# Kernel optimization log

Measured on AMD Instinct MI355X. Metric: run time of the kernel, lower is better.

## Reference

```python
import jax, jax.numpy as jnp
import numpy as np
import math

HID, H = 384, 4
D = HID // H  # 96, HGT head dim
N_T = [2048, 2048, 2048, 1024, 1024]  # user_turn, ai_turn, stance, pressure, belief
OFF = [0, 2048, 4096, 6144, 7168]
NTOT = 8192
# (src_type, dst_type, num_edges)
EDGES = [(0, 1, 32768), (1, 0, 32768), (1, 2, 32768), (2, 2, 32768),
         (0, 3, 16384), (3, 1, 32768), (1, 4, 16384), (4, 2, 32768)]
E_OFF = np.concatenate([[0], np.cumsum([c for _, _, c in EDGES])]).tolist()


def _gelu(x):
    return jax.nn.gelu(x, approximate=False)


def _ln(x, g, b, eps=1e-5):
    m = x.mean(-1, keepdims=True)
    v = ((x - m) ** 2).mean(-1, keepdims=True)
    return (x - m) * jax.lax.rsqrt(v + eps) * g + b


def _mha(q_in, kv_in, Wqkv, bqkv, Wo, bo):
    # torch nn.MultiheadAttention (batch_first, batch=1); Wqkv stored [E, 3E]
    E = HID
    q = (q_in @ Wqkv[:, :E] + bqkv[:E]).reshape(-1, H, D)
    k = (kv_in @ Wqkv[:, E:2 * E] + bqkv[E:2 * E]).reshape(-1, H, D)
    v = (kv_in @ Wqkv[:, 2 * E:] + bqkv[2 * E:]).reshape(-1, H, D)
    s = jnp.einsum('qhd,khd->hqk', q, k) / math.sqrt(D)
    w = jax.nn.softmax(s, axis=-1)
    o = jnp.einsum('hqk,khd->qhd', w, v).reshape(-1, E)
    return o @ Wo + bo


def _forward(x_user, x_ai, x_stance, x_pressure, x_belief,
             hgt_Wkqv, hgt_bkqv, hgt_Wout, hgt_bout, hgt_krel, hgt_vrel, hgt_prel, hgt_skip,
             ln_g, ln_b, sp_W, sp_b, sp_lng, sp_lnb, fc0_W, fc0_b, bn_g, bn_b,
             tq_W, tq_b, tk_W, tk_b, tv_W, tv_b, mha_Wqkv, mha_bqkv, mha_Wo, mha_bo,
             c1_W, c1_b, c2_W, c2_b, op_W, op_b, as1_W, as1_b, as2_W, as2_b,
             sc1_W, sc1_b, sc2_W, sc2_b, cl1_W, cl1_b, cl_lng, cl_lnb,
             cl2_W, cl2_b, cl3_W, cl3_b, tp_W, tp_b, edge_src, edge_dst):
    xs = [x_user, x_ai, x_stance, x_pressure, x_belief]
    for l in range(2):
        kqv = [x @ hgt_Wkqv[l, t] + hgt_bkqv[l, t] for t, x in enumerate(xs)]
        kk = [a[:, :HID].reshape(-1, H, D) for a in kqv]
        qq = [a[:, HID:2 * HID].reshape(-1, H, D) for a in kqv]
        vv = [a[:, 2 * HID:].reshape(-1, H, D) for a in kqv]
        al, msg, dgl = [], [], []
        for r, (s, d, cnt) in enumerate(EDGES):
            si = edge_src[E_OFF[r]:E_OFF[r + 1]]
            di = edge_dst[E_OFF[r]:E_OFF[r + 1]]
            ke = jnp.einsum('ehd,hdf->ehf', kk[s][si], hgt_krel[l, r])
            ve = jnp.einsum('ehd,hdf->ehf', vv[s][si], hgt_vrel[l, r])
            a = (qq[d][di] * ke).sum(-1) * hgt_prel[l, r] / math.sqrt(D)  # [E_r, H]
            al.append(a); msg.append(ve); dgl.append(di + OFF[d])
        a = jnp.concatenate(al); ve = jnp.concatenate(msg); dg = jnp.concatenate(dgl)
        mx = jax.ops.segment_max(a, dg, num_segments=NTOT)
        ex = jnp.exp(a - mx[dg])
        den = jax.ops.segment_sum(ex, dg, num_segments=NTOT)
        w = ex / den[dg]
        agg = jax.ops.segment_sum(ve * w[:, :, None], dg, num_segments=NTOT).reshape(NTOT, HID)
        new = []
        for t, x in enumerate(xs):
            o = _gelu(agg[OFF[t]:OFF[t] + N_T[t]]) @ hgt_Wout[l, t] + hgt_bout[l, t]
            g = jax.nn.sigmoid(hgt_skip[l, t])
            new.append(g * o + (1 - g) * x)
        xs = [_ln(_gelu(v), ln_g[t], ln_b[t]) for t, v in enumerate(new)]
    user_h, ai_h, stance_h, pressure_h, belief_h = xs

    # ---- StanceTrajectoryEncoder ----
    hs = _gelu(_ln(stance_h @ sp_W + sp_b, sp_lng, sp_lnb))

    def bn(x, i):  # eval-mode BatchNorm1d, running stats (0, 1)
        return x * (bn_g[i] / math.sqrt(1.0 + 1e-5)) + bn_b[i]

    xg = jax.nn.relu(bn(hs @ fc0_W + fc0_b, 0))
    Ns = hs.shape[0]
    for i in range(2):  # SGFormer TransConv layers (linear global attention)
        q = (xg @ tq_W[i] + tq_b[i]).reshape(Ns, H, HID)
        k = (xg @ tk_W[i] + tk_b[i]).reshape(Ns, H, HID)
        v = (xg @ tv_W[i] + tv_b[i]).reshape(Ns, H, HID)
        qn = q / jnp.linalg.norm(q)  # global Frobenius norm, as in SGFormer
        kn = k / jnp.linalg.norm(k)
        kvs = jnp.einsum('lhm,lhd->hmd', kn, v)
        num = jnp.einsum('nhm,hmd->nhd', qn, kvs) + Ns * v
        dnm = jnp.einsum('nhm,hm->nh', qn, kn.sum(0))[:, :, None] + Ns
        z = (num / dnm).mean(axis=1)  # mean over heads
        xg = jax.nn.relu(bn(0.5 * z + 0.5 * xg, i + 1))  # residual alpha=0.5
    h_mixed = 0.7 * hs + 0.3 * xg
    traj = _mha(h_mixed, h_mixed, mha_Wqkv[1], mha_bqkv[1], mha_Wo[1], mha_bo[1])
    traj_summary = traj.mean(0, keepdims=True)  # [1, HID]
    ci = h_mixed.T[None]  # [1, C, L]
    dn = ('NCH', 'OIH', 'NCH')
    c = jax.lax.conv_general_dilated(ci, c1_W, (1,), [(1, 1)], dimension_numbers=dn) + c1_b[None, :, None]
    c = _gelu(c)
    c = jax.lax.conv_general_dilated(c, c2_W, (1,), [(1, 1)], dimension_numbers=dn) + c2_b[None, :, None]
    c = _gelu(c)
    decay_summary = c.mean(axis=2)  # [1, HID//2]
    traj_emb = jnp.concatenate([traj_summary, decay_summary], -1) @ op_W + op_b

    # ---- PressureResponseModule ----
    ai_ctx = _mha(ai_h, user_h, mha_Wqkv[0], mha_bqkv[0], mha_Wo[0], mha_bo[0])
    ml = min(N_T[1], N_T[0])
    comb = jnp.concatenate([ai_h[:ml], user_h[:ml]], -1)
    pscores = jax.nn.sigmoid((jax.nn.relu(comb @ as1_W + as1_b) @ as2_W + as2_b)[:, 0])
    ai_pooled = ai_ctx.mean(0, keepdims=True)

    # ---- belief attention + stance comparison + classifier ----
    bctx = _mha(ai_h, belief_h, mha_Wqkv[2], mha_bqkv[2], mha_Wo[2], mha_bo[2]).mean(0, keepdims=True)
    sd_in = jnp.concatenate([stance_h[0:1], stance_h[-1:]], -1)
    stance_delta = jax.nn.relu(sd_in @ sc1_W + sc1_b) @ sc2_W + sc2_b
    comb2 = jnp.concatenate([traj_emb, ai_pooled, bctx, stance_delta], -1)  # [1, 1344]
    z = jax.nn.relu(_ln(comb2 @ cl1_W + cl1_b, cl_lng, cl_lnb))
    z = jax.nn.relu(z @ cl2_W + cl2_b)
    logits = (z @ cl3_W + cl3_b).reshape(())
    decay = jax.nn.sigmoid(logits)
    per_turn = jax.nn.sigmoid((ai_ctx @ tp_W + tp_b)[:, 0])
    return logits, decay, per_turn, pscores


def setup_inputs() -> dict:
    key = jax.random.key(0)
    ks = iter(jax.random.split(key, 128))

    def P(shape, fan_in):
        return jax.random.normal(next(ks), shape, jnp.float32) / np.float32(math.sqrt(fan_in))

    inp = {}
    for name, n in zip(['x_user', 'x_ai', 'x_stance', 'x_pressure', 'x_belief'], N_T):
        inp[name] = jax.random.normal(next(ks), (n, HID), jnp.float32)
    inp['hgt_Wkqv'] = P((2, 5, HID, 3 * HID), HID)
    inp['hgt_bkqv'] = jnp.zeros((2, 5, 3 * HID))
    inp['hgt_Wout'] = P((2, 5, HID, HID), HID)
    inp['hgt_bout'] = jnp.zeros((2, 5, HID))
    inp['hgt_krel'] = P((2, 8, H, D, D), D)
    inp['hgt_vrel'] = P((2, 8, H, D, D), D)
    inp['hgt_prel'] = jnp.ones((2, 8, H))
    inp['hgt_skip'] = jnp.ones((2, 5))
    inp['ln_g'] = jnp.ones((5, HID)); inp['ln_b'] = jnp.zeros((5, HID))
    inp['sp_W'] = P((HID, HID), HID); inp['sp_b'] = jnp.zeros((HID,))
    inp['sp_lng'] = jnp.ones((HID,)); inp['sp_lnb'] = jnp.zeros((HID,))
    inp['fc0_W'] = P((HID, HID), HID); inp['fc0_b'] = jnp.zeros((HID,))
    inp['bn_g'] = jnp.ones((3, HID)); inp['bn_b'] = jnp.zeros((3, HID))
    for nm in ['tq', 'tk', 'tv']:
        inp[nm + '_W'] = P((2, HID, H * HID), HID)
        inp[nm + '_b'] = jnp.zeros((2, H * HID))
    inp['mha_Wqkv'] = P((3, HID, 3 * HID), HID)
    inp['mha_bqkv'] = jnp.zeros((3, 3 * HID))
    inp['mha_Wo'] = P((3, HID, HID), HID)
    inp['mha_bo'] = jnp.zeros((3, HID))
    inp['c1_W'] = P((HID, HID, 3), HID * 3); inp['c1_b'] = jnp.zeros((HID,))
    inp['c2_W'] = P((HID // 2, HID, 3), HID * 3); inp['c2_b'] = jnp.zeros((HID // 2,))
    inp['op_W'] = P((HID + HID // 2, HID), HID + HID // 2); inp['op_b'] = jnp.zeros((HID,))
    inp['as1_W'] = P((2 * HID, HID), 2 * HID); inp['as1_b'] = jnp.zeros((HID,))
    inp['as2_W'] = P((HID, 1), HID); inp['as2_b'] = jnp.zeros((1,))
    inp['sc1_W'] = P((2 * HID, HID), 2 * HID); inp['sc1_b'] = jnp.zeros((HID,))
    inp['sc2_W'] = P((HID, HID // 2), HID); inp['sc2_b'] = jnp.zeros((HID // 2,))
    CIN = 3 * HID + HID // 2
    inp['cl1_W'] = P((CIN, HID), CIN); inp['cl1_b'] = jnp.zeros((HID,))
    inp['cl_lng'] = jnp.ones((HID,)); inp['cl_lnb'] = jnp.zeros((HID,))
    inp['cl2_W'] = P((HID, HID // 2), HID); inp['cl2_b'] = jnp.zeros((HID // 2,))
    inp['cl3_W'] = P((HID // 2, 1), HID // 2); inp['cl3_b'] = jnp.zeros((1,))
    inp['tp_W'] = P((HID, 1), HID); inp['tp_b'] = jnp.zeros((1,))
    srcs, dsts = [], []
    for (s, d, cnt) in EDGES:
        srcs.append(jax.random.randint(next(ks), (cnt,), 0, N_T[s], jnp.int32))
        dsts.append(jax.random.randint(next(ks), (cnt,), 0, N_T[d], jnp.int32))
    inp['edge_src'] = jnp.concatenate(srcs)
    inp['edge_dst'] = jnp.concatenate(dsts)
    return inp


def reference(x_user, x_ai, x_stance, x_pressure, x_belief,
              hgt_Wkqv, hgt_bkqv, hgt_Wout, hgt_bout, hgt_krel, hgt_vrel, hgt_prel, hgt_skip,
              ln_g, ln_b, sp_W, sp_b, sp_lng, sp_lnb, fc0_W, fc0_b, bn_g, bn_b,
              tq_W, tq_b, tk_W, tk_b, tv_W, tv_b, mha_Wqkv, mha_bqkv, mha_Wo, mha_bo,
              c1_W, c1_b, c2_W, c2_b, op_W, op_b, as1_W, as1_b, as2_W, as2_b,
              sc1_W, sc1_b, sc2_W, sc2_b, cl1_W, cl1_b, cl_lng, cl_lnb,
              cl2_W, cl2_b, cl3_W, cl3_b, tp_W, tp_b, edge_src, edge_dst):
    return _forward(x_user, x_ai, x_stance, x_pressure, x_belief,
                    hgt_Wkqv, hgt_bkqv, hgt_Wout, hgt_bout, hgt_krel, hgt_vrel, hgt_prel, hgt_skip,
                    ln_g, ln_b, sp_W, sp_b, sp_lng, sp_lnb, fc0_W, fc0_b, bn_g, bn_b,
                    tq_W, tq_b, tk_W, tk_b, tv_W, tv_b, mha_Wqkv, mha_bqkv, mha_Wo, mha_bo,
                    c1_W, c1_b, c2_W, c2_b, op_W, op_b, as1_W, as1_b, as2_W, as2_b,
                    sc1_W, sc1_b, sc2_W, sc2_b, cl1_W, cl1_b, cl_lng, cl_lnb,
                    cl2_W, cl2_b, cl3_W, cl3_b, tp_W, tp_b, edge_src, edge_dst)
```

## Files before the change

### kernel.cpp

```cpp
#include <hip/hip_runtime.h>
#include <hip/hip_bf16.h>

#define NEDGE 229376
#define NTOT  8192
#define BNCONST 0.9999950000374997f
#define ISQ96   0.10206207261596575f

__constant__ int c_NT[5]     = {2048,2048,2048,1024,1024};
__constant__ int c_OFFS[5]   = {0,2048,4096,6144,7168};
__constant__ int c_ESRC[8]   = {0,1,1,2,0,3,1,4};
__constant__ int c_EDST[8]   = {1,0,2,2,3,1,4,2};
__constant__ int c_EOFF[9]   = {0,32768,65536,98304,131072,147456,180224,196608,229376};
__constant__ int c_RELROW[8] = {0,2048,4096,6144,8192,10240,11264,13312};

static const int h_NT[5]   = {2048,2048,2048,1024,1024};
static const int h_OFFS[5] = {0,2048,4096,6144,7168};

__device__ inline float gelu_f(float x){ return 0.5f*x*(1.0f+erff(x*0.70710678118654752f)); }
__device__ inline float sigm(float x){ return 1.0f/(1.0f+expf(-x)); }
__device__ inline float wsum64(float v){
  #pragma unroll
  for (int s=32;s>0;s>>=1) v += __shfl_xor(v, s, 64);
  return v;
}
__device__ inline unsigned encf(float f){
  unsigned b = __float_as_uint(f);
  return (b & 0x80000000u) ? ~b : (b | 0x80000000u);
}
__device__ inline float decf(unsigned u){
  unsigned b = (u & 0x80000000u) ? (u & 0x7FFFFFFFu) : ~u;
  return __uint_as_float(b);
}
__device__ inline int row_type(int row){
  return (row<2048)?0:((row<4096)?1:((row<6144)?2:((row<7168)?3:4)));
}
__device__ inline float rgmax(float v){
  v = fmaxf(v, __shfl_xor(v, 1, 64));
  v = fmaxf(v, __shfl_xor(v, 2, 64));
  v = fmaxf(v, __shfl_xor(v, 4, 64));
  v = fmaxf(v, __shfl_xor(v, 8, 64));
  return v;
}
__device__ inline float rgsum(float v){
  v += __shfl_xor(v, 1, 64);
  v += __shfl_xor(v, 2, 64);
  v += __shfl_xor(v, 4, 64);
  v += __shfl_xor(v, 8, 64);
  return v;
}


__global__ void k_mix(const float* __restrict__ a, const float* __restrict__ b,
                      float* __restrict__ c, int n, float fa, float fb){
  int i = blockIdx.x*256 + threadIdx.x;
  if (i < n) c[i] = fa*a[i] + fb*b[i];
}

__global__ void k_comb(const float* __restrict__ ai, const float* __restrict__ user,
                       float* __restrict__ cb){
  int i = blockIdx.x*256 + threadIdx.x;
  if (i >= 2048*768) return;
  int n = i / 768, c = i - n*768;
  cb[i] = (c < 384) ? ai[n*384 + c] : user[n*384 + (c-384)];
}


__global__ void k_edge_pre(const int* __restrict__ esrc, const int* __restrict__ edst,
                           int* edg, int* esr, int* erl, int* cnt){
  int e = blockIdx.x*256 + threadIdx.x;
  if (e >= NEDGE) return;
  int r = 0;
  #pragma unroll
  for (int q=1;q<8;q++) if (e >= c_EOFF[q]) r = q;
  int dg = c_OFFS[c_EDST[r]] + edst[e];
  edg[e] = dg;
  esr[e] = c_RELROW[r] + esrc[e];
  erl[e] = r;
  atomicAdd(&cnt[dg], 1);
}

__global__ __launch_bounds__(1024) void k_scan(const int* __restrict__ cnt, int* __restrict__ off){
  __shared__ int sh[1024];
  int tid = threadIdx.x;
  int base = tid*8;
  int loc[8]; int run = 0;
  #pragma unroll
  for (int i=0;i<8;i++){ loc[i] = run; run += cnt[base+i]; }
  sh[tid] = run;
  __syncthreads();
  for (int d=1; d<1024; d<<=1){
    int v = (tid >= d) ? sh[tid-d] : 0;
    __syncthreads();
    sh[tid] += v;
    __syncthreads();
  }
  int pre = (tid==0) ? 0 : sh[tid-1];
  #pragma unroll
  for (int i=0;i<8;i++) off[base+i] = pre + loc[i];
  if (tid==1023) off[8192] = sh[1023];
}

__global__ void k_scatter(const int* __restrict__ edg, const int* __restrict__ off,
                          int* cnt2, int* csr){
  int e = blockIdx.x*256 + threadIdx.x;
  if (e >= NEDGE) return;
  int dg = edg[e];
  int pos = off[dg] + atomicAdd(&cnt2[dg], 1);
  csr[pos] = e;
}


__global__ __launch_bounds__(256) void gemm_f(
    const float* __restrict__ A, int lda, const float* __restrict__ B, int ldb,
    const float* __restrict__ bias, const float* __restrict__ cs, const float* __restrict__ csh,
    float kmul, float* __restrict__ C, int ldc, int M, int N, int K, int act, int agelu)
{
  __shared__ float As[2][16][68];
  __shared__ float Bs[2][16][68];
  int tid = threadIdx.x;
  int tx = tid & 15, ty = tid >> 4;
  int am = tid >> 2, ak = (tid & 3) * 4;
  int bk = tid >> 4, bn = (tid & 15) * 4;
  int m0 = blockIdx.y * 64, n0 = blockIdx.x * 64;
  int gmA = m0 + am;
  int gnB = n0 + bn;
  int ntiles = K >> 4;
  float4 ra, rb;
  float acc[4][4] = {};

  auto fetch = [&](int kk){
    if (gmA < M){
      ra = *reinterpret_cast<const float4*>(&A[(size_t)gmA*lda + kk + ak]);
      if (agelu){ ra.x=gelu_f(ra.x); ra.y=gelu_f(ra.y); ra.z=gelu_f(ra.z); ra.w=gelu_f(ra.w); }
    } else ra = make_float4(0.f,0.f,0.f,0.f);
    if (gnB + 3 < N){
      rb = *reinterpret_cast<const float4*>(&B[(size_t)(kk + bk)*ldb + gnB]);
    } else {
      rb.x = (gnB   < N) ? B[(size_t)(kk + bk)*ldb + gnB  ] : 0.f;
      rb.y = (gnB+1 < N) ? B[(size_t)(kk + bk)*ldb + gnB+1] : 0.f;
      rb.z = (gnB+2 < N) ? B[(size_t)(kk + bk)*ldb + gnB+2] : 0.f;
      rb.w = (gnB+3 < N) ? B[(size_t)(kk + bk)*ldb + gnB+3] : 0.f;
    }
  };
  auto stage = [&](int b){
    As[b][ak  ][am] = ra.x;
    As[b][ak+1][am] = ra.y;
    As[b][ak+2][am] = ra.z;
    As[b][ak+3][am] = ra.w;
    *reinterpret_cast<float4*>(&Bs[b][bk][bn]) = rb;
  };

  fetch(0);
  stage(0);
  __syncthreads();
  for (int t = 0; t < ntiles; t++){
    int cur = t & 1;
    if (t + 1 < ntiles) fetch((t+1) << 4);
    #pragma unroll
    for (int k = 0; k < 16; k++) {
      float4 a4 = *reinterpret_cast<const float4*>(&As[cur][k][ty*4]);
      float4 b4 = *reinterpret_cast<const float4*>(&Bs[cur][k][tx*4]);
      float a[4] = {a4.x, a4.y, a4.z, a4.w};
      float b[4] = {b4.x, b4.y, b4.z, b4.w};
      #pragma unroll
      for (int i=0;i<4;i++)
        #pragma unroll
        for (int j=0;j<4;j++) acc[i][j] += a[i]*b[j];
    }
    if (t + 1 < ntiles) stage(cur ^ 1);
    __syncthreads();
  }
  #pragma unroll
  for (int i=0;i<4;i++){
    int gm = m0 + ty*4 + i; if (gm >= M) continue;
    #pragma unroll
    for (int j=0;j<4;j++){
      int gn = n0 + tx*4 + j; if (gn >= N) continue;
      float v = acc[i][j];
      if (bias) v += bias[gn];
      float s = kmul;
      if (cs) s *= cs[gn];
      v *= s;
      if (csh) v += csh[gn];
      if (act==1) v = fmaxf(v, 0.f);
      else if (act==2) v = gelu_f(v);
      C[(size_t)gm*ldc + gn] = v;
    }
  }
}

__global__ __launch_bounds__(256) void gemm_rel(
    const float* __restrict__ KQV_, const float* __restrict__ krel_l,
    const float* __restrict__ vrel_l, float* __restrict__ KE_, float* __restrict__ VE_)
{
  int z = blockIdx.z;
  int w = z & 1, h = (z >> 1) & 3, r = z >> 3;
  int s = c_ESRC[r];
  int Ns = c_NT[s];
  int m0 = blockIdx.y * 64;
  if (m0 >= Ns) return;
  int n0 = blockIdx.x * 64;
  const float* A = KQV_ + (size_t)c_OFFS[s]*1152 + (w ? 768 : 0) + h*96;
  const float* B = (w ? vrel_l : krel_l) + (size_t)(r*4 + h)*9216;
  float* C = (w ? VE_ : KE_) + (size_t)c_RELROW[r]*384 + h*96;

  __shared__ float As[2][16][68];
  __shared__ float Bs[2][16][68];
  int tid = threadIdx.x;
  int tx = tid & 15, ty = tid >> 4;
  int am = tid >> 2, ak = (tid & 3) * 4;
  int bk = tid >> 4, bn = (tid & 15) * 4;
  int gmA = m0 + am;
  int gnB = n0 + bn;
  float4 ra, rb;
  float acc[4][4] = {};

  auto fetch = [&](int kk){
    ra = (gmA < Ns) ? *reinterpret_cast<const float4*>(&A[(size_t)gmA*1152 + kk + ak])
                    : make_float4(0.f,0.f,0.f,0.f);
    if (gnB + 3 < 96){
      rb = *reinterpret_cast<const float4*>(&B[(size_t)(kk + bk)*96 + gnB]);
    } else {
      rb.x = (gnB   < 96) ? B[(size_t)(kk + bk)*96 + gnB  ] : 0.f;
      rb.y = (gnB+1 < 96) ? B[(size_t)(kk + bk)*96 + gnB+1] : 0.f;
      rb.z = (gnB+2 < 96) ? B[(size_t)(kk + bk)*96 + gnB+2] : 0.f;
      rb.w = (gnB+3 < 96) ? B[(size_t)(kk + bk)*96 + gnB+3] : 0.f;
    }
  };
  auto stage = [&](int b){
    As[b][ak  ][am] = ra.x;
    As[b][ak+1][am] = ra.y;
    As[b][ak+2][am] = ra.z;
    As[b][ak+3][am] = ra.w;
    *reinterpret_cast<float4*>(&Bs[b][bk][bn]) = rb;
  };

  fetch(0);
  stage(0);
  __syncthreads();
  for (int t = 0; t < 6; t++){
    int cur = t & 1;
    if (t + 1 < 6) fetch((t+1) << 4);
    #pragma unroll
    for (int k = 0; k < 16; k++) {
      float4 a4 = *reinterpret_cast<const float4*>(&As[cur][k][ty*4]);
      float4 b4 = *reinterpret_cast<const float4*>(&Bs[cur][k][tx*4]);
      float a[4] = {a4.x, a4.y, a4.z, a4.w};
      float b[4] = {b4.x, b4.y, b4.z, b4.w};
      #pragma unroll
      for (int i=0;i<4;i++)
        #pragma unroll
        for (int j=0;j<4;j++) acc[i][j] += a[i]*b[j];
    }
    if (t + 1 < 6) stage(cur ^ 1);
    __syncthreads();
  }
  #pragma unroll
  for (int i=0;i<4;i++){
    int gm = m0 + ty*4 + i; if (gm >= Ns) continue;
    #pragma unroll
    for (int j=0;j<4;j++){
      int gn = n0 + tx*4 + j; if (gn >= 96) continue;
      C[(size_t)gm*384 + gn] = acc[i][j];
    }
  }
}

__global__ __launch_bounds__(256) void gemm_atb_ks(
    const float* __restrict__ A0, int lda, const float* __restrict__ B0, int ldb,
    float* __restrict__ C0, int ldc, int M, int N, int L,
    int hsA, int hsB, int hsC, int nch)
{
  __shared__ float As[2][16][68];
  __shared__ float Bs[2][16][68];
  int h = blockIdx.z / nch, c = blockIdx.z % nch;
  const float* A = A0 + (size_t)h*hsA;
  const float* B = B0 + (size_t)h*hsB;
  float* C = C0 + (size_t)h*hsC;
  int l0 = c*256;
  int tid = threadIdx.x;
  int tx = tid & 15, ty = tid >> 4;
  int sl = tid >> 4, sq = (tid & 15) * 4;
  int m0 = blockIdx.y * 64, n0 = blockIdx.x * 64;
  int gmA = m0 + sq, gnB = n0 + sq;
  int ntiles = 16;
  float4 ra, rb;
  float acc[4][4] = {};

  auto fetch = [&](int ll){
    if (gmA + 3 < M){
      ra = *reinterpret_cast<const float4*>(&A[(size_t)(ll + sl)*lda + gmA]);
    } else {
      ra.x = (gmA   < M) ? A[(size_t)(ll + sl)*lda + gmA  ] : 0.f;
      ra.y = (gmA+1 < M) ? A[(size_t)(ll + sl)*lda + gmA+1] : 0.f;
      ra.z = (gmA+2 < M) ? A[(size_t)(ll + sl)*lda + gmA+2] : 0.f;
      ra.w = (gmA+3 < M) ? A[(size_t)(ll + sl)*lda + gmA+3] : 0.f;
    }
    if (gnB + 3 < N){
      rb = *reinterpret_cast<const float4*>(&B[(size_t)(ll + sl)*ldb + gnB]);
    } else {
      rb.x = (gnB   < N) ? B[(size_t)(ll + sl)*ldb + gnB  ] : 0.f;
      rb.y = (gnB+1 < N) ? B[(size_t)(ll + sl)*ldb + gnB+1] : 0.f;
      rb.z = (gnB+2 < N) ? B[(size_t)(ll + sl)*ldb + gnB+2] : 0.f;
      rb.w = (gnB+3 < N) ? B[(size_t)(ll + sl)*ldb + gnB+3] : 0.f;
    }
  };
  auto stage = [&](int b){
    *reinterpret_cast<float4*>(&As[b][sl][sq]) = ra;
    *reinterpret_cast<float4*>(&Bs[b][sl][sq]) = rb;
  };

  fetch(l0);
  stage(0);
  __syncthreads();
  for (int t = 0; t < ntiles; t++){
    int cur = t & 1;
    if (t + 1 < ntiles) fetch(l0 + ((t+1) << 4));
    #pragma unroll
    for (int l = 0; l < 16; l++) {
      float4 a4 = *reinterpret_cast<const float4*>(&As[cur][l][ty*4]);
      float4 b4 = *reinterpret_cast<const float4*>(&Bs[cur][l][tx*4]);
      float a[4] = {a4.x, a4.y, a4.z, a4.w};
      float b[4] = {b4.x, b4.y, b4.z, b4.w};
      #pragma unroll
      for (int i=0;i<4;i++)
        #pragma unroll
        for (int j=0;j<4;j++) acc[i][j] += a[i]*b[j];
    }
    if (t + 1 < ntiles) stage(cur ^ 1);
    __syncthreads();
  }
  #pragma unroll
  for (int i=0;i<4;i++){
    int gm = m0 + ty*4 + i; if (gm >= M) continue;
    #pragma unroll
    for (int j=0;j<4;j++){
      int gn = n0 + tx*4 + j; if (gn >= N) continue;
      atomicAdd(&C[(size_t)gm*ldc + gn], acc[i][j]);
    }
  }
}

__global__ __launch_bounds__(256) void fa_kernel(
    const float* __restrict__ MQ, int nq, float* __restrict__ OP, float* __restrict__ ML)
{
  __shared__ float Qs[96][68];
  __shared__ float Ksf[96][36];
  __shared__ float Vs[32][104];
  __shared__ float Ps[64][36];
  int tid = threadIdx.x;
  int tx = tid & 15, ty = tid >> 4;
  int q0 = blockIdx.x * 64;
  int h = blockIdx.y;
  int z = blockIdx.z, nch = gridDim.z;
  int kvbase = z * 512;

  #pragma unroll
  for (int i = 0; i < 6; i++){
    int e = tid + i*256;
    int r = e & 63, kq = (e >> 6) * 4;
    float4 f = *reinterpret_cast<const float4*>(&MQ[(size_t)(q0+r)*1152 + h*96 + kq]);
    Qs[kq  ][r] = f.x;
    Qs[kq+1][r] = f.y;
    Qs[kq+2][r] = f.z;
    Qs[kq+3][r] = f.w;
  }

  float m_i[4], l_i[4], acc[4][6];
  #pragma unroll
  for (int i=0;i<4;i++){
    m_i[i] = -3.0e38f; l_i[i] = 0.f;
    #pragma unroll
    for (int c=0;c<6;c++) acc[i][c] = 0.f;
  }
  int c0 = tx*6;
  __syncthreads();

  for (int t = 0; t < 16; t++){
    int kv0 = kvbase + t*32;
    #pragma unroll
    for (int i = 0; i < 3; i++){
      int e = tid + i*256;
      int n = e & 31, kq = (e >> 5) * 4;
      float4 f = *reinterpret_cast<const float4*>(&MQ[(size_t)(kv0+n)*1152 + 384 + h*96 + kq]);
      Ksf[kq  ][n] = f.x;
      Ksf[kq+1][n] = f.y;
      Ksf[kq+2][n] = f.z;
      Ksf[kq+3][n] = f.w;
      int nv = e / 24, cq = (e - nv*24) * 4;
      float4 g = *reinterpret_cast<const float4*>(&MQ[(size_t)(kv0+nv)*1152 + 768 + h*96 + cq]);
      *reinterpret_cast<float4*>(&Vs[nv][cq]) = g;
    }
    __syncthreads();

    float s0[4] = {0,0,0,0}, s1[4] = {0,0,0,0};
    #pragma unroll 8
    for (int k = 0; k < 96; k++){
      float4 a4 = *reinterpret_cast<const float4*>(&Qs[k][ty*4]);
      float2 b2 = *reinterpret_cast<const float2*>(&Ksf[k][tx*2]);
      s0[0] += a4.x*b2.x; s1[0] += a4.x*b2.y;
      s0[1] += a4.y*b2.x; s1[1] += a4.y*b2.y;
      s0[2] += a4.z*b2.x; s1[2] += a4.z*b2.y;
      s0[3] += a4.w*b2.x; s1[3] += a4.w*b2.y;
    }
    #pragma unroll
    for (int i=0;i<4;i++){
      float a = s0[i]*ISQ96, b = s1[i]*ISQ96;
      float rm = rgmax(fmaxf(a, b));
      float mn = fmaxf(m_i[i], rm);
      float alpha = expf(m_i[i] - mn);
      float p0 = expf(a - mn), p1 = expf(b - mn);
      float rs = rgsum(p0 + p1);
      l_i[i] = l_i[i]*alpha + rs;
      m_i[i] = mn;
      #pragma unroll
      for (int c=0;c<6;c++) acc[i][c] *= alpha;
      Ps[ty*4+i][tx*2  ] = p0;
      Ps[ty*4+i][tx*2+1] = p1;
    }
    __syncthreads();
    for (int kv = 0; kv < 32; kv++){
      float2 v01 = *reinterpret_cast<const float2*>(&Vs[kv][c0]);
      float2 v23 = *reinterpret_cast<const float2*>(&Vs[kv][c0+2]);
      float2 v45 = *reinterpret_cast<const float2*>(&Vs[kv][c0+4]);
      #pragma unroll
      for (int i=0;i<4;i++){
        float p = Ps[ty*4+i][kv];
        acc[i][0] += p*v01.x; acc[i][1] += p*v01.y;
        acc[i][2] += p*v23.x; acc[i][3] += p*v23.y;
        acc[i][4] += p*v45.x; acc[i][5] += p*v45.y;
      }
    }
    __syncthreads();
  }

  size_t base = ((size_t)(h*nch + z)*nq + q0);
  #pragma unroll
  for (int i=0;i<4;i++){
    size_t row = base + ty*4 + i;
    #pragma unroll
    for (int c=0;c<6;c++) OP[row*96 + c0 + c] = acc[i][c];
    if (tx == 0){
      ML[row*2  ] = m_i[i];
      ML[row*2+1] = l_i[i];
    }
  }
}

__global__ void k_famerge(const float* __restrict__ OP, const float* __restrict__ ML,
                          float* __restrict__ AO_, int nq, int nch){
  int e = blockIdx.x*256 + threadIdx.x;
  int total = 4*nq*96;
  if (e >= total) return;
  int c = e % 96;
  int q = (e / 96) % nq;
  int h = e / (96*nq);
  float M = -3.0e38f;
  for (int z = 0; z < nch; z++)
    M = fmaxf(M, ML[((size_t)(h*nch+z)*nq + q)*2]);
  float L = 0.f, O = 0.f;
  for (int z = 0; z < nch; z++){
    size_t row = (size_t)(h*nch+z)*nq + q;
    float w = expf(ML[row*2] - M);
    L += ML[row*2+1]*w;
    O += OP[row*96 + c]*w;
  }
  AO_[(size_t)q*384 + h*96 + c] = O / L;
}

__global__ void k_im2col(const float* __restrict__ in, float* __restrict__ imc){
  int e = blockIdx.x*256 + threadIdx.x;
  if (e >= 2048*1152) return;
  int p = e / 1152, k = e - p*1152;
  int ic = k / 3, j = k - ic*3;
  int gp = p - 1 + j;
  imc[e] = (gp >= 0 && gp < 2048) ? in[(size_t)gp*384 + ic] : 0.f;
}
__global__ void k_wtr(const float* __restrict__ W, float* __restrict__ WT, int OC){
  int e = blockIdx.x*256 + threadIdx.x;
  if (e >= OC*1152) return;
  int oc = e / 1152, k = e - oc*1152;
  WT[(size_t)k*OC + oc] = W[e];
}


__global__ __launch_bounds__(256) void k_escore(
    const float* __restrict__ KQV_, const float* __restrict__ KE_,
    const int* __restrict__ edg, const int* __restrict__ esr, const int* __restrict__ erl,
    const float* __restrict__ prel_l, float* __restrict__ EA)
// ... 68 lines not shown
    const float* __restrict__ O, float* __restrict__ X,
    const float* __restrict__ skip_l, const float* __restrict__ lng, const float* __restrict__ lnb)
{
  __shared__ float red[2];
  int row = blockIdx.x, tid = threadIdx.x;
  int t = row_type(row);
  float gt = sigm(skip_l[t]);
  const float* o = O + (size_t)row*384;
  float* x = X + (size_t)row*384;
  float v0 = gelu_f(gt*o[tid]     + (1.f-gt)*x[tid]);
  float v1 = gelu_f(gt*o[tid+128] + (1.f-gt)*x[tid+128]);
  float v2 = gelu_f(gt*o[tid+256] + (1.f-gt)*x[tid+256]);
  int lane = tid & 63, wid = tid >> 6;
  float s = wsum64(v0+v1+v2);
  if (lane==0) red[wid] = s;
  __syncthreads();
  float mean = (red[0]+red[1]) * (1.0f/384.0f);
  __syncthreads();
  float d0=v0-mean, d1=v1-mean, d2=v2-mean;
  float q = wsum64(d0*d0+d1*d1+d2*d2);
  if (lane==0) red[wid] = q;
  __syncthreads();
  float var = (red[0]+red[1]) * (1.0f/384.0f);
  float rs = 1.0f/sqrtf(var + 1e-5f);
  const float* g = lng + (size_t)t*384;
  const float* b = lnb + (size_t)t*384;
  x[tid]     = d0*rs*g[tid]     + b[tid];
  x[tid+128] = d1*rs*g[tid+128] + b[tid+128];
  x[tid+256] = d2*rs*g[tid+256] + b[tid+256];
}

__global__ __launch_bounds__(128) void k_lnrow(
    const float* __restrict__ X, float* __restrict__ Y,
    const float* __restrict__ g, const float* __restrict__ b, int act)
{
  __shared__ float red[2];
  int row = blockIdx.x, tid = threadIdx.x;
  const float* x = X + (size_t)row*384;
  float* y = Y + (size_t)row*384;
  float v0 = x[tid], v1 = x[tid+128], v2 = x[tid+256];
  int lane = tid & 63, wid = tid >> 6;
  float s = wsum64(v0+v1+v2);
  if (lane==0) red[wid] = s;
  __syncthreads();
  float mean = (red[0]+red[1]) * (1.0f/384.0f);
  __syncthreads();
  float d0=v0-mean, d1=v1-mean, d2=v2-mean;
  float q = wsum64(d0*d0+d1*d1+d2*d2);
  if (lane==0) red[wid] = q;
  __syncthreads();
  float var = (red[0]+red[1]) * (1.0f/384.0f);
  float rs = 1.0f/sqrtf(var + 1e-5f);
  float u0 = d0*rs*g[tid]     + b[tid];
  float u1 = d1*rs*g[tid+128] + b[tid+128];
  float u2 = d2*rs*g[tid+256] + b[tid+256];
  if (act==1){ u0=fmaxf(u0,0.f); u1=fmaxf(u1,0.f); u2=fmaxf(u2,0.f); }
  else       { u0=gelu_f(u0); u1=gelu_f(u1); u2=gelu_f(u2); }
  y[tid] = u0; y[tid+128] = u1; y[tid+256] = u2;
}


__global__ __launch_bounds__(256) void k_sumsq(const float* __restrict__ x, int n, float* out){
  __shared__ float red[4];
  float s = 0.f;
  for (int i = blockIdx.x*256 + threadIdx.x; i < n; i += gridDim.x*256){ float v=x[i]; s += v*v; }
  s = wsum64(s);
  int lane = threadIdx.x & 63, wid = threadIdx.x >> 6;
  if (lane==0) red[wid] = s;
  __syncthreads();
  if (threadIdx.x==0) atomicAdd(out, red[0]+red[1]+red[2]+red[3]);
}

__global__ void k_colsum(const float* __restrict__ A, int R, int C, float scale,
                         float* __restrict__ out){
  int col = blockIdx.x*256 + threadIdx.x;
  if (col >= C) return;
  int nchunk = gridDim.y;
  int chunk = (R + nchunk - 1)/nchunk;
  int r0 = blockIdx.y*chunk, r1 = min(R, r0+chunk);
  float s = 0.f;
  for (int r=r0; r<r1; r++) s += A[(size_t)r*C + col];
  atomicAdd(&out[col], s*scale);
}

__global__ __launch_bounds__(256) void k_dnm(const float* __restrict__ QB,
    const float* __restrict__ KSUM, const float* __restrict__ sqsk, float* __restrict__ DNM){
  int wv = blockIdx.x*4 + (threadIdx.x>>6);
  int n = wv >> 2, h = wv & 3;
  int lane = threadIdx.x & 63;
  const float* q = QB + (size_t)n*1536 + h*384;
  const float* ks = KSUM + h*384;
  float p = 0.f;
  #pragma unroll
  for (int d=lane; d<384; d+=64) p += q[d]*ks[d];
  p = wsum64(p);
  if (lane==0) DNM[n*4+h] = p * (1.0f/sqrtf(sqsk[0]*sqsk[1])) + 2048.0f;
}

__global__ void k_zcomb(const float* __restrict__ ZN, const float* __restrict__ VB_,
                        const float* __restrict__ DNM_, const float* __restrict__ sqsk,
                        float* __restrict__ XG_,
                        const float* __restrict__ bng, const float* __restrict__ bnb){
  int i = blockIdx.x*256 + threadIdx.x;
  if (i >= 2048*384) return;
  int n = i / 384, c = i - n*384;
  float inv_s = 1.0f/sqrtf(sqsk[0]*sqsk[1]);
  float zm = 0.f;
  #pragma unroll
  for (int h=0;h<4;h++){
    float num = ZN[(size_t)n*1536 + h*384 + c]*inv_s + 2048.0f*VB_[(size_t)n*1536 + h*384 + c];
    zm += num / DNM_[n*4+h];
  }
  zm *= 0.25f;
  float y = 0.5f*zm + 0.5f*XG_[i];
  y = y * (bng[c] * BNCONST) + bnb[c];
  XG_[i] = fmaxf(y, 0.f);
}


__global__ __launch_bounds__(256) void k_gemv_ks(
    const float* __restrict__ in, int K, const float* __restrict__ W, int ldw,
    float* __restrict__ tmp, int N)
{
  int c = blockIdx.x*64 + (threadIdx.x & 63);
  int w = threadIdx.x >> 6;
  int kch = blockIdx.y, nk = gridDim.y;
  int k0 = (int)(((long long)K * kch) / nk);
  int k1 = (int)(((long long)K * (kch+1)) / nk);
  float s = 0.f;
  if (c < N){
    for (int k = k0 + w; k < k1; k += 4)
      s += in[k] * W[(size_t)k*ldw + c];
  }
  __shared__ float red[4][64];
  red[w][threadIdx.x & 63] = s;
  __syncthreads();
  if (w == 0 && c < N){
    int l = threadIdx.x & 63;
    tmp[(size_t)kch*N + c] = red[0][l] + red[1][l] + red[2][l] + red[3][l];
  }
}

__global__ void k_gemv_fin(const float* __restrict__ tmp, int nk,
                           const float* __restrict__ b, float* __restrict__ out, int N, int act){
  int c = blockIdx.x*256 + threadIdx.x;
  if (c >= N) return;
  float v = 0.f;
  for (int i = 0; i < nk; i++) v += tmp[(size_t)i*N + c];
  v += b[c];
  if (act==1) v = fmaxf(v, 0.f);
  out[c] = v;
}

__global__ __launch_bounds__(256) void k_rowdot(const float* __restrict__ A, int lda, int K,
    const float* __restrict__ w, const float* __restrict__ b, float* __restrict__ out, int M){
  int r = blockIdx.x*4 + (threadIdx.x>>6);
  if (r >= M) return;
  int lane = threadIdx.x & 63;
  const float* a = A + (size_t)r*lda;
  float p = 0.f;
  for (int k = lane; k < K; k += 64) p += a[k]*w[k];
  p = wsum64(p);
  if (lane==0) out[r] = sigm(p + b[0]);
}

__global__ __launch_bounds__(64) void k_final(const float* __restrict__ z2,
    const float* __restrict__ w, const float* __restrict__ b, float* __restrict__ out){
  int lane = threadIdx.x;
  float p = 0.f;
  for (int k = lane; k < 192; k += 64) p += z2[k]*w[k];
  p = wsum64(p);
  if (lane==0){
    float l = p + b[0];
    out[0] = l;
    out[1] = sigm(l);
  }
}


extern "C" void kernel_launch(void* const* d_in, const int* in_sizes, int n_in,
                              void* d_out, int out_size, void* d_ws, size_t ws_size,
                              hipStream_t stream)
{
  const float* xin[5] = {(const float*)d_in[0], (const float*)d_in[1], (const float*)d_in[2],
                         (const float*)d_in[3], (const float*)d_in[4]};
  const float* Wkqv=(const float*)d_in[5];  const float* bkqv=(const float*)d_in[6];
  const float* Wout=(const float*)d_in[7];  const float* bout=(const float*)d_in[8];
  const float* krel=(const float*)d_in[9];  const float* vrel=(const float*)d_in[10];
  const float* prel=(const float*)d_in[11]; const float* skp =(const float*)d_in[12];
  const float* lng =(const float*)d_in[13]; const float* lnb =(const float*)d_in[14];
  const float* sp_W=(const float*)d_in[15]; const float* sp_b=(const float*)d_in[16];
  const float* sp_lng=(const float*)d_in[17]; const float* sp_lnb=(const float*)d_in[18];
  const float* fc0_W=(const float*)d_in[19]; const float* fc0_b=(const float*)d_in[20];
  const float* bn_g=(const float*)d_in[21]; const float* bn_b=(const float*)d_in[22];
  const float* tq_W=(const float*)d_in[23]; const float* tq_b=(const float*)d_in[24];
  const float* tk_W=(const float*)d_in[25]; const float* tk_b=(const float*)d_in[26];
  const float* tv_W=(const float*)d_in[27]; const float* tv_b=(const float*)d_in[28];
  const float* mWqkv=(const float*)d_in[29]; const float* mbqkv=(const float*)d_in[30];
  const float* mWo=(const float*)d_in[31];  const float* mbo=(const float*)d_in[32];
  const float* c1W=(const float*)d_in[33];  const float* c1b=(const float*)d_in[34];
  const float* c2W=(const float*)d_in[35];  const float* c2b=(const float*)d_in[36];
  const float* opW=(const float*)d_in[37];  const float* opb=(const float*)d_in[38];
  const float* as1W=(const float*)d_in[39]; const float* as1b=(const float*)d_in[40];
  const float* as2W=(const float*)d_in[41]; const float* as2b=(const float*)d_in[42];
  const float* sc1W=(const float*)d_in[43]; const float* sc1b=(const float*)d_in[44];
  const float* sc2W=(const float*)d_in[45]; const float* sc2b=(const float*)d_in[46];
  const float* cl1W=(const float*)d_in[47]; const float* cl1b=(const float*)d_in[48];
  const float* cllng=(const float*)d_in[49]; const float* cllnb=(const float*)d_in[50];
  const float* cl2W=(const float*)d_in[51]; const float* cl2b=(const float*)d_in[52];
  const float* cl3W=(const float*)d_in[53]; const float* cl3b=(const float*)d_in[54];
  const float* tpW=(const float*)d_in[55];  const float* tpb=(const float*)d_in[56];
  const int* e_src=(const int*)d_in[57];  const int* e_dst=(const int*)d_in[58];
  float* out = (float*)d_out;

  char* ws = (char*)d_ws;
  size_t off_b = 0;
  auto alloc = [&](size_t bytes)->char*{
    char* r = ws + off_b;
    off_b = (off_b + bytes + 255) & ~(size_t)255;
    return r;
  };
  float* X    = (float*)alloc((size_t)8192*384*4);
  float* KQV  = (float*)alloc((size_t)8192*1152*4);
  float* KE   = (float*)alloc((size_t)14336*384*4);
  float* VE   = (float*)alloc((size_t)14336*384*4);
  float* AGG  = (float*)alloc((size_t)8192*384*4);
  float* EA   = (float*)alloc((size_t)NEDGE*4*4);
  int* edg    = (int*)alloc((size_t)NEDGE*4);
  int* esr    = (int*)alloc((size_t)NEDGE*4);
  int* erl    = (int*)alloc((size_t)NEDGE*4);
  int* csr    = (int*)alloc((size_t)NEDGE*4);
  int* cnt    = (int*)alloc(8192*4);
  int* cnt2   = (int*)alloc(8192*4);
  int* coff   = (int*)alloc(8193*4);
  unsigned* EMX = (unsigned*)alloc(8192*4*4);
  float* EDEN = (float*)alloc(8192*4*4);
  float* SM   = (float*)alloc(65536);
  float* GT   = (float*)alloc(20*384*4);
  if (off_b > ws_size) return;

  float* SQSK = SM;
  float* TRAJSUM = SM + 8;
  float* DECAYSUM = SM + 392;
  float* TEMB = SM + 600;
  float* AIPOOL = SM + 984;
  float* BCTXV = SM + 1368;
  float* SDELT = SM + 1752;
  float* SDIN = SM + 2048;
  float* T1   = SM + 2816;
  float* Z1   = SM + 3200;
  float* Zb   = SM + 3584;
  float* Z2   = SM + 3968;
  float* KSUM = SM + 4224;
  float* DNM  = SM + 6144;

  float* QB = KQV;
  float* KB = KQV + (size_t)2048*1536;
  float* VB = KQV + (size_t)2*2048*1536;
  float* MQKV = KQV;
  float* AO = KQV + (size_t)2*2048*1536;
  float* ZNUM = KE;
  float* OWT = KE;
  float* OPART = KE;
  float* MLBUF = KE + (size_t)3200000;
  float* IMC = KE;
  float* WT  = KE + (size_t)2400000;
  float* HS = VE;
  float* XG = VE + (size_t)2048*384;
  float* HM = VE + (size_t)2*2048*384;
  float* C1O = VE + (size_t)3*2048*384;
  float* TRAJ = VE + (size_t)4*2048*384;
  float* AICTX = VE + (size_t)5*2048*384;
  float* C2O = VE + (size_t)6*2048*384;
  float* TMPA = AGG;
  float* CB = AGG;
  float* PT = AGG + (size_t)2048*768;
  float* KVS = AGG + (size_t)2048*1152;

  dim3 B256(256);
  auto gemm = [&](const float* A, int lda, const float* Bw, int ldb, const float* bias,
                  const float* cs, const float* csh, float kmul,
                  float* C, int ldc, int M, int N, int K, int act, int agelu){
    dim3 g((N+63)/64, (M+63)/64);
    gemm_f<<<g, B256, 0, stream>>>(A, lda, Bw, ldb, bias, cs, csh, kmul, C, ldc, M, N, K, act, agelu);
  };
  auto gemv = [&](const float* in, int K, const float* W, int ldw, const float* b,
                  float* o, int N, int act){
    int nk = (K + 79) / 80; if (nk > 20) nk = 20; if (nk < 1) nk = 1;
    k_gemv_ks<<<dim3((N+63)/64, nk), B256, 0, stream>>>(in, K, W, ldw, GT, N);
    k_gemv_fin<<<dim3((N+255)/256), B256, 0, stream>>>(GT, nk, b, o, N, act);
  };

  hipMemsetAsync(cnt, 0, 8192*4, stream);
  hipMemsetAsync(cnt2, 0, 8192*4, stream);
  k_edge_pre<<<dim3(NEDGE/256), B256, 0, stream>>>(e_src, e_dst, edg, esr, erl, cnt);
  k_scan<<<dim3(1), dim3(1024), 0, stream>>>(cnt, coff);
  k_scatter<<<dim3(NEDGE/256), B256, 0, stream>>>(edg, coff, cnt2, csr);

  for (int t=0;t<5;t++)
    hipMemcpyAsync(X + (size_t)h_OFFS[t]*384, xin[t], (size_t)h_NT[t]*384*4,
                   hipMemcpyDeviceToDevice, stream);

  for (int l=0;l<2;l++){
    for (int t=0;t<5;t++)
      gemm(X + (size_t)h_OFFS[t]*384, 384, Wkqv + (size_t)(l*5+t)*442368, 1152,
           bkqv + (size_t)(l*5+t)*1152, nullptr, nullptr, 1.f,
           KQV + (size_t)h_OFFS[t]*1152, 1152, h_NT[t], 1152, 384, 0, 0);
    gemm_rel<<<dim3(2,32,64), B256, 0, stream>>>(
        KQV, krel + (size_t)l*294912, vrel + (size_t)l*294912, KE, VE);
    k_escore<<<dim3(NEDGE/4), B256, 0, stream>>>(KQV, KE, edg, esr, erl, prel + (size_t)l*32, EA);
    hipMemsetAsync(EMX, 0, 8192*4*4, stream);
    hipMemsetAsync(EDEN, 0, 8192*4*4, stream);
    k_segmax<<<dim3(NEDGE*4/256), B256, 0, stream>>>(EA, edg, EMX);
    k_expsum<<<dim3(NEDGE*4/256), B256, 0, stream>>>(EA, edg, EMX, EDEN);
    k_agg<<<dim3(NTOT), dim3(128), 0, stream>>>(EA, VE, EDEN, csr, coff, esr, AGG);
    for (int t=0;t<5;t++)
      gemm(AGG + (size_t)h_OFFS[t]*384, 384, Wout + (size_t)(l*5+t)*147456, 384,
           bout + (size_t)(l*5+t)*384, nullptr, nullptr, 1.f,
           OWT + (size_t)h_OFFS[t]*384, 384, h_NT[t], 384, 384, 0, 1 );
    k_gateln<<<dim3(NTOT), dim3(128), 0, stream>>>(OWT, X, skp + l*5, lng, lnb);
  }

  const float* user_h   = X;
  const float* ai_h     = X + (size_t)2048*384;
  const float* stance_h = X + (size_t)4096*384;
  const float* belief_h = X + (size_t)7168*384;

  gemm(stance_h, 384, sp_W, 384, sp_b, nullptr, nullptr, 1.f, TMPA, 384, 2048, 384, 384, 0, 0);
  k_lnrow<<<dim3(2048), dim3(128), 0, stream>>>(TMPA, HS, sp_lng, sp_lnb, 0 );
  gemm(HS, 384, fc0_W, 384, fc0_b, bn_g, bn_b, BNCONST, XG, 384, 2048, 384, 384, 1 , 0);

  for (int i=0;i<2;i++){
    gemm(XG, 384, tq_W + (size_t)i*589824, 1536, tq_b + (size_t)i*1536, nullptr, nullptr, 1.f,
         QB, 1536, 2048, 1536, 384, 0, 0);
    gemm(XG, 384, tk_W + (size_t)i*589824, 1536, tk_b + (size_t)i*1536, nullptr, nullptr, 1.f,
         KB, 1536, 2048, 1536, 384, 0, 0);
    gemm(XG, 384, tv_W + (size_t)i*589824, 1536, tv_b + (size_t)i*1536, nullptr, nullptr, 1.f,
         VB, 1536, 2048, 1536, 384, 0, 0);
    hipMemsetAsync(SQSK, 0, 8, stream);
    k_sumsq<<<dim3(512), B256, 0, stream>>>(QB, 2048*1536, SQSK);
    k_sumsq<<<dim3(512), B256, 0, stream>>>(KB, 2048*1536, SQSK+1);
    hipMemsetAsync(KSUM, 0, 1536*4, stream);
    k_colsum<<<dim3(6,8), B256, 0, stream>>>(KB, 2048, 1536, 1.0f, KSUM);
    k_dnm<<<dim3(2048), B256, 0, stream>>>(QB, KSUM, SQSK, DNM);
    hipMemsetAsync(KVS, 0, (size_t)4*147456*4, stream);
    gemm_atb_ks<<<dim3(6,6,32), B256, 0, stream>>>(KB, 1536, VB, 1536, KVS, 384,
        384, 384, 2048, 384, 384, 147456, 8);
    for (int h=0;h<4;h++)
      gemm(QB + h*384, 1536, KVS + (size_t)h*147456, 384, nullptr, nullptr, nullptr, 1.f,
           ZNUM + h*384, 1536, 2048, 384, 384, 0, 0);
    k_zcomb<<<dim3(3072), B256, 0, stream>>>(ZNUM, VB, DNM, SQSK, XG,
        bn_g + (size_t)(i+1)*384, bn_b + (size_t)(i+1)*384);
  }

  k_mix<<<dim3(3072), B256, 0, stream>>>(HS, XG, HM, 2048*384, 0.7f, 0.3f);

  auto run_mha = [&](const float* qin, int nq, const float* kvin, int nkv, int mi, float* OUT){
    const float* Wq = mWqkv + (size_t)mi*442368;
    const float* bq = mbqkv + (size_t)mi*1152;
    gemm(qin, 384, Wq, 1152, bq, nullptr, nullptr, 1.f, MQKV, 1152, nq, 384, 384, 0, 0);
    gemm(kvin, 384, Wq + 384, 1152, bq + 384, nullptr, nullptr, 1.f, MQKV + 384, 1152, nkv, 768, 384, 0, 0);
    int nch = nkv / 512;
    fa_kernel<<<dim3(nq/64, 4, nch), B256, 0, stream>>>(MQKV, nq, OPART, MLBUF);
    k_famerge<<<dim3((4*nq*96 + 255)/256), B256, 0, stream>>>(OPART, MLBUF, AO, nq, nch);
    gemm(AO, 384, mWo + (size_t)mi*147456, 384, mbo + (size_t)mi*384,
         nullptr, nullptr, 1.f, OUT, 384, nq, 384, 384, 0, 0);
  };

  run_mha(HM, 2048, HM, 2048, 1, TRAJ);
  hipMemsetAsync(TRAJSUM, 0, 576*4, stream);
  k_colsum<<<dim3(2,8), B256, 0, stream>>>(TRAJ, 2048, 384, 1.0f/2048.0f, TRAJSUM);

  k_im2col<<<dim3(2048*1152/256), B256, 0, stream>>>(HM, IMC);
  k_wtr<<<dim3((384*1152+255)/256), B256, 0, stream>>>(c1W, WT, 384);
  gemm(IMC, 1152, WT, 384, c1b, nullptr, nullptr, 1.f, C1O, 384, 2048, 384, 1152, 2 , 0);
  k_im2col<<<dim3(2048*1152/256), B256, 0, stream>>>(C1O, IMC);
  k_wtr<<<dim3((192*1152+255)/256), B256, 0, stream>>>(c2W, WT, 192);
  gemm(IMC, 1152, WT, 192, c2b, nullptr, nullptr, 1.f, C2O, 192, 2048, 192, 1152, 2 , 0);
  k_colsum<<<dim3(1,8), B256, 0, stream>>>(C2O, 2048, 192, 1.0f/2048.0f, DECAYSUM);

  gemv(TRAJSUM, 576, opW, 384, opb, TEMB, 384, 0);

  run_mha(ai_h, 2048, user_h, 2048, 0, AICTX);
  hipMemsetAsync(AIPOOL, 0, 384*4, stream);
  k_colsum<<<dim3(2,8), B256, 0, stream>>>(AICTX, 2048, 384, 1.0f/2048.0f, AIPOOL);

  k_comb<<<dim3(6144), B256, 0, stream>>>(ai_h, user_h, CB);
  gemm(CB, 768, as1W, 384, as1b, nullptr, nullptr, 1.f, PT, 384, 2048, 384, 768, 1, 0);
  k_rowdot<<<dim3(512), B256, 0, stream>>>(PT, 384, 384, as2W, as2b, out + 2 + 2048, 2048);

  run_mha(ai_h, 2048, belief_h, 1024, 2, TRAJ);
  hipMemsetAsync(BCTXV, 0, 384*4, stream);
  k_colsum<<<dim3(2,8), B256, 0, stream>>>(TRAJ, 2048, 384, 1.0f/2048.0f, BCTXV);

  hipMemcpyAsync(SDIN, stance_h, 384*4, hipMemcpyDeviceToDevice, stream);
  hipMemcpyAsync(SDIN + 384, stance_h + (size_t)2047*384, 384*4, hipMemcpyDeviceToDevice, stream);
  gemv(SDIN, 768, sc1W, 384, sc1b, T1, 384, 1);
  gemv(T1, 384, sc2W, 192, sc2b, SDELT, 192, 0);

  gemv(TEMB, 1344, cl1W, 384, cl1b, Z1, 384, 0);
  k_lnrow<<<dim3(1), dim3(128), 0, stream>>>(Z1, Zb, cllng, cllnb, 1 );
  gemv(Zb, 384, cl2W, 192, cl2b, Z2, 192, 1);
  k_final<<<dim3(1), dim3(64), 0, stream>>>(Z2, cl3W, cl3b, out);

  k_rowdot<<<dim3(512), B256, 0, stream>>>(AICTX, 384, 384, tpW, tpb, out + 2, 2048);
}
```

Before: 3.471 ms.

## Add 128x128 register-tiled GEMM with per-row-type weight selection and batching

Introduces a gemm128 kernel with 128x128 block tiles, 8x8 per-thread accumulators, vectorized loads and stores, and z-batched or row-type-selected B/bias pointers. The five per-type KQV and output projections each collapse into one launch covering all 8192 rows, the per-head ZNUM GEMMs become one batched launch, and the transformer Q/K/V projections use the larger tile. The aim is more reuse per load and fewer launches, at the cost of higher register pressure and lower occupancy. It depends on row_type (not shown) and on 128-row tiles never straddling type boundaries.

```diff
diff --git a/kernel.cpp b/kernel.cpp
--- a/kernel.cpp
+++ b/kernel.cpp
@@ -185,6 +185,126 @@
       if (act==1) v = fmaxf(v, 0.f);
       else if (act==2) v = gelu_f(v);
       C[(size_t)gm*ldc + gn] = v;
+    }
+  }
+}
+
+__global__ __launch_bounds__(256) void gemm128(
+    const float* __restrict__ A, int lda, int sAz,
+    const float* __restrict__ B, int ldb, int sBz,
+    const float* __restrict__ bias, int sbz,
+    float* __restrict__ C, int ldc, int sCz,
+    int M, int N, int K, int act, int agelu, int tsel)
+{
+  __shared__ float As[2][16][132];
+  __shared__ float Bs[2][16][132];
+  int tid = threadIdx.x;
+  int tx = tid & 15, ty = tid >> 4;
+  int am = tid >> 1, ak = (tid & 1) * 8;
+  int bk = tid >> 4, bn = (tid & 15) * 8;
+  int m0 = blockIdx.y * 128, n0 = blockIdx.x * 128;
+  int z = blockIdx.z;
+  const float* Ab = A + (size_t)z * sAz;
+  const float* Bb = B + (size_t)z * sBz;
+  const float* bb = bias ? (bias + (size_t)z * sbz) : nullptr;
+  float* Cb = C + (size_t)z * sCz;
+  if (tsel){
+    int t = row_type(m0);
+    Bb = B + (size_t)t * sBz;
+    bb = bias ? (bias + (size_t)t * sbz) : nullptr;
+  }
+  int gmA = m0 + am, gnB = n0 + bn;
+  int ntiles = K >> 4;
+  float4 ra0, ra1, rb0, rb1;
+  float acc[8][8] = {};
+
+  auto fetch = [&](int kk){
+    if (gmA < M){
+      ra0 = *reinterpret_cast<const float4*>(&Ab[(size_t)gmA*lda + kk + ak]);
+      ra1 = *reinterpret_cast<const float4*>(&Ab[(size_t)gmA*lda + kk + ak + 4]);
+      if (agelu){
+        ra0.x=gelu_f(ra0.x); ra0.y=gelu_f(ra0.y); ra0.z=gelu_f(ra0.z); ra0.w=gelu_f(ra0.w);
+        ra1.x=gelu_f(ra1.x); ra1.y=gelu_f(ra1.y); ra1.z=gelu_f(ra1.z); ra1.w=gelu_f(ra1.w);
+      }
+    } else {
+      ra0 = make_float4(0.f,0.f,0.f,0.f); ra1 = ra0;
+    }
+    if (gnB + 7 < N){
+      rb0 = *reinterpret_cast<const float4*>(&Bb[(size_t)(kk + bk)*ldb + gnB]);
+      rb1 = *reinterpret_cast<const float4*>(&Bb[(size_t)(kk + bk)*ldb + gnB + 4]);
+    } else {
+      const float* bp = &Bb[(size_t)(kk + bk)*ldb];
+      rb0.x = (gnB   < N) ? bp[gnB  ] : 0.f;
+      rb0.y = (gnB+1 < N) ? bp[gnB+1] : 0.f;
+      rb0.z = (gnB+2 < N) ? bp[gnB+2] : 0.f;
+      rb0.w = (gnB+3 < N) ? bp[gnB+3] : 0.f;
+      rb1.x = (gnB+4 < N) ? bp[gnB+4] : 0.f;
+      rb1.y = (gnB+5 < N) ? bp[gnB+5] : 0.f;
+      rb1.z = (gnB+6 < N) ? bp[gnB+6] : 0.f;
+      rb1.w = (gnB+7 < N) ? bp[gnB+7] : 0.f;
+    }
+  };
+  auto stage = [&](int b){
+    As[b][ak  ][am] = ra0.x;
+    As[b][ak+1][am] = ra0.y;
+    As[b][ak+2][am] = ra0.z;
+    As[b][ak+3][am] = ra0.w;
+    As[b][ak+4][am] = ra1.x;
+    As[b][ak+5][am] = ra1.y;
+    As[b][ak+6][am] = ra1.z;
+    As[b][ak+7][am] = ra1.w;
+    *reinterpret_cast<float4*>(&Bs[b][bk][bn  ]) = rb0;
+    *reinterpret_cast<float4*>(&Bs[b][bk][bn+4]) = rb1;
+  };
+
+  fetch(0);
+  stage(0);
+  __syncthreads();
+  for (int t = 0; t < ntiles; t++){
+    int cur = t & 1;
+    if (t + 1 < ntiles) fetch((t+1) << 4);
+    #pragma unroll
+    for (int k = 0; k < 16; k++) {
+      float4 a0 = *reinterpret_cast<const float4*>(&As[cur][k][ty*8]);
+      float4 a1 = *reinterpret_cast<const float4*>(&As[cur][k][ty*8+4]);
+      float4 b0 = *reinterpret_cast<const float4*>(&Bs[cur][k][tx*8]);
+      float4 b1 = *reinterpret_cast<const float4*>(&Bs[cur][k][tx*8+4]);
+      float a[8] = {a0.x,a0.y,a0.z,a0.w,a1.x,a1.y,a1.z,a1.w};
+      float b[8] = {b0.x,b0.y,b0.z,b0.w,b1.x,b1.y,b1.z,b1.w};
+      #pragma unroll
+      for (int i=0;i<8;i++)
+        #pragma unroll
+        for (int j=0;j<8;j++) acc[i][j] += a[i]*b[j];
+    }
+    if (t + 1 < ntiles) stage(cur ^ 1);
+    __syncthreads();
+  }
+
+  bool fullN = (n0 + 127 < N);
+  #pragma unroll
+  for (int i=0;i<8;i++){
+    int gm = m0 + ty*8 + i; if (gm >= M) continue;
+    float v[8];
+    #pragma unroll
+    for (int j=0;j<8;j++){
+      float x = acc[i][j];
+      if (bb){
+        int gn = n0 + tx*8 + j;
+        if (gn < N) x += bb[gn];
+      }
+      if (act==1) x = fmaxf(x, 0.f);
+      else if (act==2) x = gelu_f(x);
+      v[j] = x;
+    }
+    if (fullN){
+      *reinterpret_cast<float4*>(&Cb[(size_t)gm*ldc + n0 + tx*8    ]) = make_float4(v[0],v[1],v[2],v[3]);
+      *reinterpret_cast<float4*>(&Cb[(size_t)gm*ldc + n0 + tx*8 + 4]) = make_float4(v[4],v[5],v[6],v[7]);
+    } else {
+      #pragma unroll
+      for (int j=0;j<8;j++){
+        int gn = n0 + tx*8 + j; if (gn >= N) continue;
+        Cb[(size_t)gm*ldc + gn] = v[j];
+      }
     }
   }
 }
@@ -859,10 +979,11 @@
                    hipMemcpyDeviceToDevice, stream);
 
   for (int l=0;l<2;l++){
-    for (int t=0;t<5;t++)
-      gemm(X + (size_t)h_OFFS[t]*384, 384, Wkqv + (size_t)(l*5+t)*442368, 1152,
-           bkqv + (size_t)(l*5+t)*1152, nullptr, nullptr, 1.f,
-           KQV + (size_t)h_OFFS[t]*1152, 1152, h_NT[t], 1152, 384, 0, 0);
+    gemm128<<<dim3(9, 64), B256, 0, stream>>>(
+        X, 384, 0,
+        Wkqv + (size_t)l*5*442368, 1152, 442368,
+        bkqv + (size_t)l*5*1152, 1152,
+        KQV, 1152, 0, 8192, 1152, 384, 0, 0, 1 );
     gemm_rel<<<dim3(2,32,64), B256, 0, stream>>>(
         KQV, krel + (size_t)l*294912, vrel + (size_t)l*294912, KE, VE);
     k_escore<<<dim3(NEDGE/4), B256, 0, stream>>>(KQV, KE, edg, esr, erl, prel + (size_t)l*32, EA);
@@ -871,10 +992,11 @@
     k_segmax<<<dim3(NEDGE*4/256), B256, 0, stream>>>(EA, edg, EMX);
     k_expsum<<<dim3(NEDGE*4/256), B256, 0, stream>>>(EA, edg, EMX, EDEN);
     k_agg<<<dim3(NTOT), dim3(128), 0, stream>>>(EA, VE, EDEN, csr, coff, esr, AGG);
-    for (int t=0;t<5;t++)
-      gemm(AGG + (size_t)h_OFFS[t]*384, 384, Wout + (size_t)(l*5+t)*147456, 384,
-           bout + (size_t)(l*5+t)*384, nullptr, nullptr, 1.f,
-           OWT + (size_t)h_OFFS[t]*384, 384, h_NT[t], 384, 384, 0, 1 );
+    gemm128<<<dim3(3, 64), B256, 0, stream>>>(
+        AGG, 384, 0,
+        Wout + (size_t)l*5*147456, 384, 147456,
+        bout + (size_t)l*5*384, 384,
+        OWT, 384, 0, 8192, 384, 384, 0, 1 , 1 );
     k_gateln<<<dim3(NTOT), dim3(128), 0, stream>>>(OWT, X, skp + l*5, lng, lnb);
   }
 
@@ -888,12 +1010,15 @@
   gemm(HS, 384, fc0_W, 384, fc0_b, bn_g, bn_b, BNCONST, XG, 384, 2048, 384, 384, 1 , 0);
 
   for (int i=0;i<2;i++){
-    gemm(XG, 384, tq_W + (size_t)i*589824, 1536, tq_b + (size_t)i*1536, nullptr, nullptr, 1.f,
-         QB, 1536, 2048, 1536, 384, 0, 0);
-    gemm(XG, 384, tk_W + (size_t)i*589824, 1536, tk_b + (size_t)i*1536, nullptr, nullptr, 1.f,
-         KB, 1536, 2048, 1536, 384, 0, 0);
-    gemm(XG, 384, tv_W + (size_t)i*589824, 1536, tv_b + (size_t)i*1536, nullptr, nullptr, 1.f,
-         VB, 1536, 2048, 1536, 384, 0, 0);
+    gemm128<<<dim3(12,16), B256, 0, stream>>>(
+        XG, 384, 0, tq_W + (size_t)i*589824, 1536, 0,
+        tq_b + (size_t)i*1536, 0, QB, 1536, 0, 2048, 1536, 384, 0, 0, 0);
+    gemm128<<<dim3(12,16), B256, 0, stream>>>(
+        XG, 384, 0, tk_W + (size_t)i*589824, 1536, 0,
+        tk_b + (size_t)i*1536, 0, KB, 1536, 0, 2048, 1536, 384, 0, 0, 0);
+    gemm128<<<dim3(12,16), B256, 0, stream>>>(
+        XG, 384, 0, tv_W + (size_t)i*589824, 1536, 0,
+        tv_b + (size_t)i*1536, 0, VB, 1536, 0, 2048, 1536, 384, 0, 0, 0);
     hipMemsetAsync(SQSK, 0, 8, stream);
     k_sumsq<<<dim3(512), B256, 0, stream>>>(QB, 2048*1536, SQSK);
     k_sumsq<<<dim3(512), B256, 0, stream>>>(KB, 2048*1536, SQSK+1);
@@ -903,9 +1028,9 @@
     hipMemsetAsync(KVS, 0, (size_t)4*147456*4, stream);
     gemm_atb_ks<<<dim3(6,6,32), B256, 0, stream>>>(KB, 1536, VB, 1536, KVS, 384,
         384, 384, 2048, 384, 384, 147456, 8);
-    for (int h=0;h<4;h++)
-      gemm(QB + h*384, 1536, KVS + (size_t)h*147456, 384, nullptr, nullptr, nullptr, 1.f,
-           ZNUM + h*384, 1536, 2048, 384, 384, 0, 0);
+    gemm128<<<dim3(3,16,4), B256, 0, stream>>>(
+        QB, 1536, 384, KVS, 384, 147456,
+        nullptr, 0, ZNUM, 1536, 384, 2048, 384, 384, 0, 0, 0);
     k_zcomb<<<dim3(3072), B256, 0, stream>>>(ZNUM, VB, DNM, SQSK, XG,
         bn_g + (size_t)(i+1)*384, bn_b + (size_t)(i+1)*384);
   }
```

After: 3.510 ms. About the same (+1.1%).
